# Optimization experiments

Hardware: AMD Instinct MI355X
Metric: run time of the kernel (lower is better)

## Reference

```python
import jax, jax.numpy as jnp
import numpy as np

B, S, E = 4, 4096, 1024
H, D, L = 16, 64, 64   # heads, head_dim, landmarks
KS = 33                # depthwise conv kernel size (seq dim)
N_ITER = 6


def setup_inputs() -> dict:
    key = jax.random.key(0)
    ks = jax.random.split(key, 8)
    s = 0.02
    return {
        "hidden_states": jax.random.normal(ks[0], (B, S, E), dtype=jnp.float32),
        "Wq": jax.random.normal(ks[1], (E, E), dtype=jnp.float32) * s,
        "bq": jnp.zeros((E,), dtype=jnp.float32),
        "Wk": jax.random.normal(ks[2], (E, E), dtype=jnp.float32) * s,
        "bk": jnp.zeros((E,), dtype=jnp.float32),
        "Wv": jax.random.normal(ks[3], (E, E), dtype=jnp.float32) * s,
        "bv": jnp.zeros((E,), dtype=jnp.float32),
        "conv_w": jax.random.normal(ks[4], (H, 1, KS, 1), dtype=jnp.float32) * 0.1,
    }


def _iterative_pinv_original(a, n_iter=N_ITER):
    # a: [B,H,L,L]. Faithful to _pinv_original_nystrom: GLOBAL max over all batches/heads.
    eye = jnp.eye(a.shape[-1], dtype=a.dtype)
    val = a.swapaxes(-1, -2) / jnp.max(jnp.sum(a, axis=-2))
    for _ in range(n_iter):
        kv = a @ val
        val = 0.25 * val @ (13.0 * eye - kv @ (15.0 * eye - kv @ (7.0 * eye - kv)))
    return val


def reference(hidden_states, Wq, bq, Wk, bk, Wv, bv, conv_w):
    scale = D ** -0.25  # divide q and k each by head_dim**0.25

    def heads(x):  # [B,S,E] -> [B,H,S,D]
        return x.reshape(B, S, H, D).transpose(0, 2, 1, 3)

    q = heads(hidden_states @ Wq + bq) * scale
    k = heads(hidden_states @ Wk + bk) * scale
    v = heads(hidden_states @ Wv + bv)

    # landmark means over segments of length S//L
    ql = q.reshape(B, H, L, S // L, D).mean(axis=-2)  # [B,H,L,D]
    kl = k.reshape(B, H, L, S // L, D).mean(axis=-2)  # [B,H,L,D]

    kernel_1 = jax.nn.softmax(jnp.einsum('bhsd,bhld->bhsl', q, kl), axis=-1)   # [B,H,S,L]
    kernel_2 = jax.nn.softmax(jnp.einsum('bhmd,bhld->bhml', ql, kl), axis=-1)  # [B,H,L,L]
    kernel_3 = jax.nn.softmax(jnp.einsum('bhld,bhsd->bhls', ql, k), axis=-1)   # [B,H,L,S]

    pinv = _iterative_pinv_original(kernel_2)
    attention_probs = kernel_1 @ pinv            # [B,H,S,L]
    new_value = kernel_3 @ v                     # [B,H,L,D]
    ctx = attention_probs @ new_value            # [B,H,S,D]

    # depthwise conv skip on value_layer: Conv2d(H,H,(KS,1),groups=H,bias=False)
    pad = KS // 2
    conv_out = jax.lax.conv_general_dilated(
        v, conv_w, window_strides=(1, 1), padding=((pad, pad), (0, 0)),
        dimension_numbers=('NCHW', 'OIHW', 'NCHW'), feature_group_count=H)
    ctx = ctx + conv_out

    return ctx.transpose(0, 2, 1, 3).reshape(B, S, H * D)
```

## Files before the change

### kernel.cpp

```cpp
#include <hip/hip_runtime.h>
#include <stdint.h>

typedef unsigned short u16;
typedef float f32x4 __attribute__((ext_vector_type(4)));
typedef __bf16 bf16x8 __attribute__((ext_vector_type(8)));
typedef u16 u16x8 __attribute__((ext_vector_type(8)));
typedef u16 u16x4 __attribute__((ext_vector_type(4)));

#define SCALE_QK 0.35355339059327373f

#define BAR() asm volatile("s_barrier" ::: "memory")
#define WAIT_LGKM0() do { asm volatile("s_waitcnt lgkmcnt(0)" ::: "memory"); __builtin_amdgcn_sched_barrier(0); } while (0)
#define WAIT_VM(n) do { asm volatile("s_waitcnt vmcnt(" #n ")" ::: "memory"); __builtin_amdgcn_sched_barrier(0); } while (0)

__device__ __forceinline__ u16 f2bf(float f) {
  union { float f; uint32_t u; } x; x.f = f;
  uint32_t r = x.u + 0x7fffu + ((x.u >> 16) & 1u);
  return (u16)(r >> 16);
}
__device__ __forceinline__ float bf2f(u16 h) {
  union { uint32_t u; float f; } x; x.u = ((uint32_t)h) << 16;
  return x.f;
}
__device__ __forceinline__ void gload16(const void* g, void* l) {
  __builtin_amdgcn_global_load_lds((const __attribute__((address_space(1))) void*)g,
                                   (__attribute__((address_space(3))) void*)l, 16, 0, 0);
}
__device__ __forceinline__ bf16x8 ld_f32_to_bf8(const float* p) {
  f32x4 a = *(const f32x4*)p, b = *(const f32x4*)(p + 4);
  union { u16x8 u; bf16x8 h; } c;
  c.u[0] = f2bf(a[0]); c.u[1] = f2bf(a[1]); c.u[2] = f2bf(a[2]); c.u[3] = f2bf(a[3]);
  c.u[4] = f2bf(b[0]); c.u[5] = f2bf(b[1]); c.u[6] = f2bf(b[2]); c.u[7] = f2bf(b[3]);
  return c.h;
}

__global__ __launch_bounds__(256) void k_wt(const float* __restrict__ Wq, const float* __restrict__ Wk,
                                            const float* __restrict__ Wv, u16* __restrict__ Wt) {
  __shared__ float tile[64][65];
  const int bx = blockIdx.x;
  const int w = bx >> 8, tn = (bx >> 4) & 15, tk = bx & 15;
  const float* W = (w == 0) ? Wq : ((w == 1) ? Wk : Wv);
  const int t = threadIdx.x;
  const int r = t >> 2, c0 = (t & 3) * 16;
  const float* src = W + (size_t)(tk * 64 + r) * 1024 + tn * 64 + c0;
#pragma unroll
  for (int j = 0; j < 16; j += 4) {
    f32x4 x = *(const f32x4*)(src + j);
    tile[r][c0 + j + 0] = x[0]; tile[r][c0 + j + 1] = x[1];
    tile[r][c0 + j + 2] = x[2]; tile[r][c0 + j + 3] = x[3];
  }
  __syncthreads();
  u16* dst = Wt + (size_t)(w * 1024 + tn * 64 + r) * 1024 + tk * 64 + c0;
#pragma unroll
  for (int j = 0; j < 16; ++j) dst[j] = f2bf(tile[c0 + j][r]);
}

__global__ __launch_bounds__(256) void k_hb(const float* __restrict__ in, u16* __restrict__ out) {
  const size_t i = ((size_t)blockIdx.x * 256 + threadIdx.x) * 8;
  f32x4 v0 = *(const f32x4*)(in + i);
  f32x4 v1 = *(const f32x4*)(in + i + 4);
  u16x8 o;
  o[0] = f2bf(v0[0]); o[1] = f2bf(v0[1]); o[2] = f2bf(v0[2]); o[3] = f2bf(v0[3]);
  o[4] = f2bf(v1[0]); o[5] = f2bf(v1[1]); o[6] = f2bf(v1[2]); o[7] = f2bf(v1[3]);
  *(u16x8*)(out + i) = o;
}

__device__ __forceinline__ bf16x8 frg(const u16* buf, int row, int ks, int lhi) {
  const int ck = (ks << 2) + lhi;
  return *reinterpret_cast<const bf16x8*>(buf + (row << 6) + ((ck ^ (row & 7)) << 3));
}
__device__ __forceinline__ void issue(const u16* g, int rowbase, int tc, u16* ldsbase, int wid) {
  gload16(g + (((size_t)rowbase) << 10) + tc, ldsbase + ((rowbase + (wid << 3)) << 6));
}
template <int Q>
__device__ __forceinline__ void quad_mfma(const bf16x8 (&af)[2][2], const bf16x8 (&bf)[4][2],
                                          f32x4 (&acc)[8][4]) {
#pragma unroll
  for (int mm = 0; mm < 2; ++mm)
#pragma unroll
    for (int n = 0; n < 4; ++n) {
      acc[Q * 2 + mm][n] = __builtin_amdgcn_mfma_f32_16x16x32_bf16(af[mm][0], bf[n][0], acc[Q * 2 + mm][n], 0, 0, 0);
      acc[Q * 2 + mm][n] = __builtin_amdgcn_mfma_f32_16x16x32_bf16(af[mm][1], bf[n][1], acc[Q * 2 + mm][n], 0, 0, 0);
    }
}
#define LOADA_TO(dst, Q)                                     \
  dst[0][0] = frg(ASr, rA0 + (Q)*32, 0, lhi);                \
  dst[0][1] = frg(ASr, rA0 + (Q)*32, 1, lhi);                \
  dst[1][0] = frg(ASr, rA0 + (Q)*32 + 16, 0, lhi);           \
  dst[1][1] = frg(ASr, rA0 + (Q)*32 + 16, 1, lhi);

__global__ __launch_bounds__(512) void k_gemm2(const u16* __restrict__ A, const u16* __restrict__ Bt,
                                               const float* __restrict__ bq, const float* __restrict__ bk,
                                               const float* __restrict__ bv,
                                               u16* __restrict__ oq, u16* __restrict__ ok, u16* __restrict__ ov,
                                               float* __restrict__ ql, float* __restrict__ kl) {
  __shared__ __align__(16) u16 AS[2][256 * 64];
  __shared__ __align__(16) u16 BS[2][256 * 64];
  __shared__ __align__(16) u16 obuf[8][16][70];
  const int t = threadIdx.x, lane = t & 63, wid = t >> 6;
  const int wm = wid >> 2, wn = wid & 3;
  const int bm = blockIdx.x, bn = blockIdx.y;
  const int l15 = lane & 15, lhi = lane >> 4;

  const int rowoff = t >> 3;
  const int cswz = (t & 7) ^ (rowoff & 7);
  const u16* aG = A + (((size_t)(bm * 256 + rowoff)) << 10) + (cswz << 3);
  const u16* bG = Bt + (((size_t)(bn * 256 + rowoff)) << 10) + (cswz << 3);

  const int rA0 = wm * 128 + l15;
  const int rB0 = wn * 64 + l15;

  f32x4 acc[8][4];
#pragma unroll
  for (int m = 0; m < 8; ++m)
#pragma unroll
    for (int n = 0; n < 4; ++n) acc[m][n] = (f32x4){0.f, 0.f, 0.f, 0.f};

  issue(bG, 0, 0, BS[0], wid);
  issue(bG, 64, 0, BS[0], wid);
  issue(bG, 128, 0, BS[0], wid);
  issue(bG, 192, 0, BS[0], wid);
  issue(aG, 0, 0, AS[0], wid);
  issue(aG, 128, 0, AS[0], wid);
  issue(aG, 64, 0, AS[0], wid);
  issue(aG, 192, 0, AS[0], wid);
  WAIT_VM(0);
  BAR();

  for (int u = 0; u < 15; ++u) {
    const int pu = u & 1;
    const u16* ASr = AS[pu];
    const u16* BSr = BS[pu];
    u16* ASw = AS[pu ^ 1];
    u16* BSw = BS[pu ^ 1];
    const int tc = (u + 1) << 6;
    bf16x8 bfr[4][2];
    bf16x8 afA[2][2], afB[2][2];
#pragma unroll
    for (int n = 0; n < 4; ++n) {
      bfr[n][0] = frg(BSr, rB0 + n * 16, 0, lhi);
      bfr[n][1] = frg(BSr, rB0 + n * 16, 1, lhi);
    }
    LOADA_TO(afA, 0)
    LOADA_TO(afB, 1)
    issue(bG, 0, tc, BSw, wid);
    issue(bG, 64, tc, BSw, wid);
    issue(bG, 128, tc, BSw, wid);
    issue(bG, 192, tc, BSw, wid);
    issue(aG, 0, tc, ASw, wid);
    issue(aG, 128, tc, ASw, wid);
    __builtin_amdgcn_s_setprio(1);
    quad_mfma<0>(afA, bfr, acc);
    __builtin_amdgcn_s_setprio(0);
    LOADA_TO(afA, 2)
    issue(aG, 64, tc, ASw, wid);
    issue(aG, 192, tc, ASw, wid);
    __builtin_amdgcn_s_setprio(1);
    quad_mfma<1>(afB, bfr, acc);
    __builtin_amdgcn_s_setprio(0);
    LOADA_TO(afB, 3)
    __builtin_amdgcn_s_setprio(1);
    quad_mfma<2>(afA, bfr, acc);
    __builtin_amdgcn_s_setprio(0);
    __builtin_amdgcn_s_setprio(1);
    quad_mfma<3>(afB, bfr, acc);
    __builtin_amdgcn_s_setprio(0);
    WAIT_VM(0);
    BAR();
  }
  {
    const u16* ASr = AS[1];
    const u16* BSr = BS[1];
    bf16x8 bfr[4][2];
    bf16x8 afA[2][2], afB[2][2];
#pragma unroll
    for (int n = 0; n < 4; ++n) {
      bfr[n][0] = frg(BSr, rB0 + n * 16, 0, lhi);
      bfr[n][1] = frg(BSr, rB0 + n * 16, 1, lhi);
    }
    LOADA_TO(afA, 0)
    LOADA_TO(afB, 1)
    quad_mfma<0>(afA, bfr, acc);
    LOADA_TO(afA, 2)
    quad_mfma<1>(afB, bfr, acc);
    LOADA_TO(afB, 3)
    quad_mfma<2>(afA, bfr, acc);
    quad_mfma<3>(afB, bfr, acc);
  }

  const int which = bn >> 2;
  const float* bias = (which == 0) ? bq : ((which == 1) ? bk : bv);
  u16* op = (which == 0) ? oq : ((which == 1) ? ok : ov);
  const float scl = (which < 2) ? SCALE_QK : 1.0f;
  const int h = ((bn & 3) << 2) + wn;
  const int rowBase2 = (bm << 8) + (wm << 7);
  const int rl = lhi << 2;
  const int srow = lane >> 2, d0 = (lane & 3) * 16;
  float bb[4];
#pragma unroll
  for (int n = 0; n < 4; ++n) bb[n] = bias[((bn & 3) << 8) + (wn << 6) + n * 16 + l15];
#pragma unroll
  for (int m = 0; m < 8; ++m) {
#pragma unroll
    for (int n = 0; n < 4; ++n)
#pragma unroll
      for (int r = 0; r < 4; ++r)
        obuf[wid][rl + r][n * 16 + l15] = f2bf((acc[m][n][r] + bb[n]) * scl);
    const int gm = rowBase2 + m * 16 + srow;
    const int b_ = gm >> 12, s = gm & 4095;
    u16* dst = op + (((size_t)b_ * 16 + h) * 4096 + s) * 64 + d0;
    *(u16x8*)dst = *(const u16x8*)&obuf[wid][srow][d0];
    *(u16x8*)(dst + 8) = *(const u16x8*)&obuf[wid][srow][d0 + 8];
  }
  if (which < 2) {
    float* lmp = (which == 0) ? ql : kl;
    const int bh = ((bm >> 4) << 4) + h;
#pragma unroll
    for (int sg = 0; sg < 2; ++sg) {
#pragma unroll
      for (int n = 0; n < 4; ++n) {
        float s = 0.f;
#pragma unroll
        for (int mi = 0; mi < 4; ++mi)
#pragma unroll
          for (int r = 0; r < 4; ++r) s += (acc[sg * 4 + mi][n][r] + bb[n]) * scl;
        s += __shfl_xor(s, 16, 64);
        s += __shfl_xor(s, 32, 64);
        if (lhi == 0) {
          const int lseg = ((bm & 15) << 2) + (wm << 1) + sg;
          lmp[(size_t)bh * 4096 + lseg * 64 + n * 16 + l15] = s * 0.015625f;
        }
      }
    }
  }
}

__global__ __launch_bounds__(256) void k_k2(const float* __restrict__ ql, const float* __restrict__ kl,
                                            float* __restrict__ k2t, float* __restrict__ colmax,
                                            u16* __restrict__ klb) {
  __shared__ __align__(16) float qlT[64 * 68];
  __shared__ __align__(16) float klT[64 * 68];
  __shared__ __align__(16) float sc[64 * 68];
  const int bh = blockIdx.x, t = threadIdx.x;
  {
    const int r = t >> 2, c0 = (t & 3) * 16;
    const float* qp = ql + (size_t)bh * 4096 + r * 64 + c0;
    const float* kp = kl + (size_t)bh * 4096 + r * 64 + c0;
    u16* kb_ = klb + (size_t)bh * 4096 + r * 64 + c0;
#pragma unroll
    for (int j = 0; j < 16; ++j) {
      qlT[(c0 + j) * 68 + r] = qp[j];
      const float kv = kp[j];
      klT[(c0 + j) * 68 + r] = kv;
      kb_[j] = f2bf(kv);
    }
  }
  __syncthreads();
  {
    const int mg = (t >> 4) * 4, lg = (t & 15) * 4;
    float acc[4][4];
#pragma unroll
    for (int i = 0; i < 4; ++i)
#pragma unroll
      for (int j = 0; j < 4; ++j) acc[i][j] = 0.f;
    for (int d0 = 0; d0 < 64; ++d0) {
      f32x4 x = *(const f32x4*)&qlT[d0 * 68 + mg];
      f32x4 y = *(const f32x4*)&klT[d0 * 68 + lg];
#pragma unroll
      for (int i = 0; i < 4; ++i)
#pragma unroll
        for (int j = 0; j < 4; ++j) acc[i][j] += x[i] * y[j];
    }
#pragma unroll
    for (int i = 0; i < 4; ++i)
#pragma unroll
      for (int j = 0; j < 4; ++j) sc[(mg + i) * 68 + lg + j] = acc[i][j];
  }
  __syncthreads();
  if (t < 64) {
    float mx = -1e30f;
    for (int l = 0; l < 64; ++l) mx = fmaxf(mx, sc[t * 68 + l]);
    float sum = 0.f;
    for (int l = 0; l < 64; ++l) { float e = __expf(sc[t * 68 + l] - mx); sc[t * 68 + l] = e; sum += e; }
    const float inv = 1.0f / sum;
    for (int l = 0; l < 64; ++l) sc[t * 68 + l] *= inv;
  }
  __syncthreads();
  {
    const int r = t >> 2, c0 = (t & 3) * 16;
    float* ot = k2t + (size_t)bh * 4096 + r * 64 + c0;
#pragma unroll
    for (int j = 0; j < 16; ++j) ot[j] = sc[(c0 + j) * 68 + r];
  }
  if (t < 64) {
    float s = 0.f;
    for (int m = 0; m < 64; ++m) s += sc[m * 68 + t];
    for (int off = 32; off; off >>= 1) s = fmaxf(s, __shfl_down(s, off, 64));
    if (t == 0) colmax[bh] = s;
  }
}

__global__ __launch_bounds__(64) void k_max(const float* __restrict__ colmax, float* __restrict__ gmax) {
  const int t = threadIdx.x;
  float v = colmax[t];
  for (int off = 32; off; off >>= 1) v = fmaxf(v, __shfl_down(v, off, 64));
  if (t == 0) *gmax = v;
}

__global__ __launch_bounds__(512) void k_pinv(const float* __restrict__ k2t, const float* __restrict__ gmaxp,
                                              float* __restrict__ pinv) {
  __shared__ float valN[4096];
  __shared__ float kvT[4096];
  __shared__ float t1N[4096];
  __shared__ float t2N[4096];
  const int bh = blockIdx.x, t = threadIdx.x;
  const float* aT = k2t + (size_t)bh * 4096;
  const float ginv = 1.0f / gmaxp[0];
  const int rt = t >> 3, ct0 = (t & 7) * 8;
  {
    const float* p = aT + rt * 64 + ct0;
#pragma unroll
    for (int j = 0; j < 8; ++j) valN[rt * 64 + ct0 + j] = p[j] * ginv;
  }
  __syncthreads();
  const int rg = (t >> 4) * 2, cg = (t & 15) * 4;
  float acc[2][4];
  for (int it = 0; it < 6; ++it) {
#pragma unroll
    for (int i = 0; i < 2; ++i)
#pragma unroll
      for (int j = 0; j < 4; ++j) acc[i][j] = 0.f;
    for (int k = 0; k < 64; ++k) {
      const float x0 = aT[k * 64 + rg], x1 = aT[k * 64 + rg + 1];
      f32x4 y = *(const f32x4*)&valN[k * 64 + cg];
#pragma unroll
      for (int j = 0; j < 4; ++j) { acc[0][j] += x0 * y[j]; acc[1][j] += x1 * y[j]; }
    }
#pragma unroll
    for (int i = 0; i < 2; ++i)
#pragma unroll
      for (int j = 0; j < 4; ++j) kvT[(cg + j) * 64 + rg + i] = acc[i][j];
    __syncthreads();
#pragma unroll
    for (int j = 0; j < 8; ++j) {
      const int c = ct0 + j;
      t1N[rt * 64 + c] = ((rt == c) ? 7.0f : 0.0f) - kvT[c * 64 + rt];
    }
    __syncthreads();
#pragma unroll
    for (int i = 0; i < 2; ++i)
#pragma unroll
      for (int j = 0; j < 4; ++j) acc[i][j] = 0.f;
    for (int k = 0; k < 64; ++k) {
      const float x0 = kvT[k * 64 + rg], x1 = kvT[k * 64 + rg + 1];
      f32x4 y = *(const f32x4*)&t1N[k * 64 + cg];
#pragma unroll
      for (int j = 0; j < 4; ++j) { acc[0][j] += x0 * y[j]; acc[1][j] += x1 * y[j]; }
    }
#pragma unroll
    for (int i = 0; i < 2; ++i)
#pragma unroll
      for (int j = 0; j < 4; ++j) {
        const int r_ = rg + i, c_ = cg + j;
        t2N[r_ * 64 + c_] = ((r_ == c_) ? 15.0f : 0.0f) - acc[i][j];
      }
    __syncthreads();
#pragma unroll
    for (int i = 0; i < 2; ++i)
#pragma unroll
      for (int j = 0; j < 4; ++j) acc[i][j] = 0.f;
    for (int k = 0; k < 64; ++k) {
      const float x0 = kvT[k * 64 + rg], x1 = kvT[k * 64 + rg + 1];
      f32x4 y = *(const f32x4*)&t2N[k * 64 + cg];
#pragma unroll
      for (int j = 0; j < 4; ++j) { acc[0][j] += x0 * y[j]; acc[1][j] += x1 * y[j]; }
    }
#pragma unroll
    for (int i = 0; i < 2; ++i)
#pragma unroll
      for (int j = 0; j < 4; ++j) {
        const int r_ = rg + i, c_ = cg + j;
        t1N[r_ * 64 + c_] = ((r_ == c_) ? 13.0f : 0.0f) - acc[i][j];
      }
    __syncthreads();
#pragma unroll
    for (int j = 0; j < 8; ++j) t2N[(ct0 + j) * 64 + rt] = valN[rt * 64 + ct0 + j];
    __syncthreads();
#pragma unroll
    for (int i = 0; i < 2; ++i)
#pragma unroll
      for (int j = 0; j < 4; ++j) acc[i][j] = 0.f;
    for (int k = 0; k < 64; ++k) {
      const float x0 = t2N[k * 64 + rg], x1 = t2N[k * 64 + rg + 1];
      f32x4 y = *(const f32x4*)&t1N[k * 64 + cg];
#pragma unroll
      for (int j = 0; j < 4; ++j) { acc[0][j] += x0 * y[j]; acc[1][j] += x1 * y[j]; }
    }
#pragma unroll
    for (int i = 0; i < 2; ++i)
#pragma unroll
      for (int j = 0; j < 4; ++j) valN[(rg + i) * 64 + cg + j] = 0.25f * acc[i][j];
    __syncthreads();
  }
  {
    float* o = pinv + (size_t)bh * 4096 + rt * 64 + ct0;
#pragma unroll
    for (int j = 0; j < 8; ++j) o[j] = valN[rt * 64 + ct0 + j];
  }
}

__global__ __launch_bounds__(256) void k_s3nv(const float* __restrict__ ql, const u16* __restrict__ kb,
                                              const u16* __restrict__ vb,
                                              float* __restrict__ nvp, float* __restrict__ zp) {
  __shared__ __align__(16) u16 VT[64][72];
  __shared__ __align__(16) u16 e_lds[4][16][72];
  const int bh = blockIdx.x, scn = blockIdx.y;
  const int t = threadIdx.x, lane = t & 63, w = t >> 6;
  const int l15 = lane & 15, kg = (lane >> 4) << 3, rl = (lane >> 4) << 2;
  const float* aRow = ql + (size_t)bh * 4096 + (w * 16 + l15) * 64 + kg;
  bf16x8 aql[2];
  aql[0] = ld_f32_to_bf8(aRow);
  aql[1] = ld_f32_to_bf8(aRow + 32);
  f32x4 accv[4];
#pragma unroll
  for (int n = 0; n < 4; ++n) accv[n] = (f32x4){0.f, 0.f, 0.f, 0.f};
  float zacc[4] = {0.f, 0.f, 0.f, 0.f};

  for (int sub = 0; sub < 16; ++sub) {
    const int s0 = scn * 1024 + sub * 64;
    __syncthreads();
    {
      const u16* vp = vb + ((size_t)bh * 4096 + s0 + lane) * 64 + w * 16;
      u16x8 h0 = *(const u16x8*)vp, h1 = *(const u16x8*)(vp + 8);
#pragma unroll
      for (int j = 0; j < 8; ++j) { VT[w * 16 + j][lane] = h0[j]; VT[w * 16 + 8 + j][lane] = h1[j]; }
    }
    __syncthreads();
    const u16* bRow = kb + ((size_t)bh * 4096 + s0 + l15) * 64 + kg;
    f32x4 e[4];
#pragma unroll
    for (int n = 0; n < 4; ++n) e[n] = (f32x4){0.f, 0.f, 0.f, 0.f};
#pragma unroll
    for (int ks = 0; ks < 2; ++ks)
#pragma unroll
      for (int n = 0; n < 4; ++n) {
        bf16x8 bk = *reinterpret_cast<const bf16x8*>(bRow + n * 1024 + ks * 32);
        e[n] = __builtin_amdgcn_mfma_f32_16x16x32_bf16(aql[ks], bk, e[n], 0, 0, 0);
      }
#pragma unroll
    for (int n = 0; n < 4; ++n)
#pragma unroll
      for (int r = 0; r < 4; ++r) {
        const float v = __expf(e[n][r]);
        zacc[r] += v;
        e_lds[w][rl + r][n * 16 + l15] = f2bf(v);
      }
    WAIT_LGKM0();
#pragma unroll
    for (int ks = 0; ks < 2; ++ks) {
      bf16x8 af = *reinterpret_cast<const bf16x8*>(&e_lds[w][l15][kg + ks * 32]);
#pragma unroll
      for (int n = 0; n < 4; ++n) {
        bf16x8 bf_ = *reinterpret_cast<const bf16x8*>(&VT[n * 16 + l15][kg + ks * 32]);
        accv[n] = __builtin_amdgcn_mfma_f32_16x16x32_bf16(af, bf_, accv[n], 0, 0, 0);
      }
    }
  }
#pragma unroll
  for (int r = 0; r < 4; ++r)
#pragma unroll
    for (int n = 0; n < 4; ++n)
      nvp[(((size_t)scn * 64 + bh) * 64 + w * 16 + rl + r) * 64 + n * 16 + l15] = accv[n][r];
#pragma unroll
  for (int r = 0; r < 4; ++r) {
    float s = zacc[r];
    s += __shfl_xor(s, 1, 64); s += __shfl_xor(s, 2, 64);
    s += __shfl_xor(s, 4, 64); s += __shfl_xor(s, 8, 64);
    if (l15 == 0) zp[((size_t)scn * 64 + bh) * 64 + w * 16 + rl + r] = s;
  }
}

__global__ __launch_bounds__(256) void k_pnv(const float* __restrict__ pinv, const float* __restrict__ nvp,
                                             const float* __restrict__ zp, u16* __restrict__ Mtb) {
  __shared__ __align__(16) float XT[64 * 68];
  __shared__ __align__(16) float Y[64 * 68];
  const int bh = blockIdx.x, t = threadIdx.x;
  {
    const int r = t >> 2, c0 = (t & 3) * 16;
    const float* pp = pinv + (size_t)bh * 4096 + r * 64 + c0;
#pragma unroll
    for (int j = 0; j < 16; ++j) XT[(c0 + j) * 68 + r] = pp[j];
    float zs = 0.f;
#pragma unroll
    for (int p = 0; p < 4; ++p) zs += zp[((size_t)p * 64 + bh) * 64 + r];
    const float iz = 1.0f / zs;
#pragma unroll
    for (int j = 0; j < 16; ++j) {
      float s = 0.f;
#pragma unroll
      for (int p = 0; p < 4; ++p) s += nvp[(((size_t)p * 64 + bh) * 64 + r) * 64 + c0 + j];
      Y[r * 68 + c0 + j] = s * iz;
    }
  }
  __syncthreads();
  const int rg = (t >> 4) * 4, cg = (t & 15) * 4;
  float acc[4][4];
#pragma unroll
  for (int i = 0; i < 4; ++i)
#pragma unroll
    for (int j = 0; j < 4; ++j) acc[i][j] = 0.f;
  for (int k = 0; k < 64; ++k) {
    f32x4 x = *(const f32x4*)&XT[k * 68 + rg];
    f32x4 y = *(const f32x4*)&Y[k * 68 + cg];
#pragma unroll
    for (int i = 0; i < 4; ++i)
#pragma unroll
      for (int j = 0; j < 4; ++j) acc[i][j] += x[i] * y[j];
  }
#pragma unroll
  for (int j = 0; j < 4; ++j) {
    u16x4 o = {f2bf(acc[0][j]), f2bf(acc[1][j]), f2bf(acc[2][j]), f2bf(acc[3][j])};
    *(u16x4*)&Mtb[(size_t)bh * 4096 + (cg + j) * 64 + rg] = o;
  }
}

__global__ __launch_bounds__(256) void k_out(const u16* __restrict__ qb, const u16* __restrict__ vb,
                                             const u16* __restrict__ klb, const u16* __restrict__ Mtb,
                                             const float* __restrict__ cw, float* __restrict__ out) {
  __shared__ __align__(16) u16 P_lds[4][16][72];
  __shared__ __align__(16) u16 vtile_t[64][100];
  __shared__ float wsh[33];
  const int bid = blockIdx.x;
  const int bh = bid >> 6, st = bid & 63;
  const int b = bh >> 4, h = bh & 15;
  const int t = threadIdx.x, lane = t & 63, w = t >> 6;
  const int sbase = st * 64;
  const int l15 = lane & 15, kg = (lane >> 4) << 3, rl = (lane >> 4) << 2;

  if (t < 33) wsh[t] = cw[h * 33 + t];
  for (int idx = t; idx < 96 * 8; idx += 256) {
    const int row = idx >> 3, c8 = idx & 7;
    const int sg = sbase + row - 16;
    u16x8 val = {0, 0, 0, 0, 0, 0, 0, 0};
    if (sg >= 0 && sg < 4096) val = *(const u16x8*)(vb + ((size_t)bh * 4096 + sg) * 64 + c8 * 8);
#pragma unroll
    for (int j = 0; j < 8; ++j) vtile_t[c8 * 8 + j][row] = val[j];
  }

  f32x4 c1[4];
#pragma unroll
  for (int n = 0; n < 4; ++n) c1[n] = (f32x4){0.f, 0.f, 0.f, 0.f};
  {
    const u16* aRow = qb + ((size_t)bh * 4096 + sbase + w * 16 + l15) * 64 + kg;
    const u16* kRow = klb + (size_t)bh * 4096 + l15 * 64 + kg;
#pragma unroll
    for (int ks = 0; ks < 2; ++ks) {
      bf16x8 af = *reinterpret_cast<const bf16x8*>(aRow + ks * 32);
#pragma unroll
      for (int n = 0; n < 4; ++n) {
        bf16x8 bf_ = *reinterpret_cast<const bf16x8*>(kRow + n * 1024 + ks * 32);
        c1[n] = __builtin_amdgcn_mfma_f32_16x16x32_bf16(af, bf_, c1[n], 0, 0, 0);
      }
    }
  }
  float invZ[4];
  {
    float z[4] = {0.f, 0.f, 0.f, 0.f};
#pragma unroll
    for (int n = 0; n < 4; ++n)
#pragma unroll
      for (int r = 0; r < 4; ++r) { float v = __expf(c1[n][r]); c1[n][r] = v; z[r] += v; }
#pragma unroll
    for (int r = 0; r < 4; ++r) {
      float s = z[r];
      s += __shfl_xor(s, 1, 64); s += __shfl_xor(s, 2, 64);
      s += __shfl_xor(s, 4, 64); s += __shfl_xor(s, 8, 64);
      invZ[r] = 1.0f / s;
    }
#pragma unroll
    for (int n = 0; n < 4; ++n)
#pragma unroll
      for (int r = 0; r < 4; ++r)
        P_lds[w][rl + r][n * 16 + l15] = f2bf(c1[n][r]);
  }
  __syncthreads();
  f32x4 c2[4];
#pragma unroll
  for (int n = 0; n < 4; ++n) c2[n] = (f32x4){0.f, 0.f, 0.f, 0.f};
  {
    const u16* mRow = Mtb + (size_t)bh * 4096 + l15 * 64 + kg;
#pragma unroll
    for (int ks = 0; ks < 2; ++ks) {
      bf16x8 af = *reinterpret_cast<const bf16x8*>(&P_lds[w][l15][kg + ks * 32]);
#pragma unroll
      for (int n = 0; n < 4; ++n) {
        bf16x8 bf_ = *reinterpret_cast<const bf16x8*>(mRow + n * 1024 + ks * 32);
        c2[n] = __builtin_amdgcn_mfma_f32_16x16x32_bf16(af, bf_, c2[n], 0, 0, 0);
      }
    }
  }
  const int base = w * 16 + rl;
#pragma unroll
  for (int n = 0; n < 4; ++n) {
    const int d = n * 16 + l15;
    float vcol[36];
#pragma unroll
    for (int k8 = 0; k8 < 9; ++k8) {
      u16x4 vq = *(const u16x4*)&vtile_t[d][base + k8 * 4];
      vcol[k8 * 4 + 0] = bf2f(vq[0]); vcol[k8 * 4 + 1] = bf2f(vq[1]);
      vcol[k8 * 4 + 2] = bf2f(vq[2]); vcol[k8 * 4 + 3] = bf2f(vq[3]);
    }
    float cv[4] = {0.f, 0.f, 0.f, 0.f};
#pragma unroll
    for (int jt = 0; jt < 33; ++jt) {
      const float ww = wsh[jt];
#pragma unroll
      for (int r = 0; r < 4; ++r) cv[r] += ww * vcol[r + jt];
    }
#pragma unroll
    for (int r = 0; r < 4; ++r) {
      const int sgl = sbase + base + r;
      out[((size_t)b * 4096 + sgl) * 1024 + h * 64 + d] = c2[n][r] * invZ[r] + cv[r];
    }
  }
}

extern "C" void kernel_launch(void* const* d_in, const int* in_sizes, int n_in,
                              void* d_out, int out_size, void* d_ws, size_t ws_size,
                              hipStream_t stream) {
  const float* hidden = (const float*)d_in[0];
  const float* Wq = (const float*)d_in[1];
  const float* bq = (const float*)d_in[2];
  const float* Wk = (const float*)d_in[3];
  const float* bk = (const float*)d_in[4];
  const float* Wv = (const float*)d_in[5];
  const float* bv = (const float*)d_in[6];
  const float* cw = (const float*)d_in[7];
  float* out = (float*)d_out;

  char* ws = (char*)d_ws;
  u16* qb = (u16*)(ws);
  u16* kb = (u16*)(ws + 33554432ull);
  u16* vb = (u16*)(ws + 67108864ull);
  float* ql = (float*)(ws + 100663296ull);
  float* kl = (float*)(ws + 101711872ull);
  float* k2t = (float*)(ws + 102760448ull);
  float* pinvb = (float*)(ws + 103809024ull);
  float* nvp = (float*)(ws + 104857600ull);
  float* zp = (float*)(ws + 109051904ull);
  u16* Mtb = (u16*)(ws + 109117440ull);
  u16* klb = (u16*)(ws + 109641728ull);
  float* stats = (float*)(ws + 110690304ull);
  u16* wt = (u16*)(ws + 110694400ull);
  u16* hb = (u16*)(ws + 116985856ull);

  k_wt<<<768, 256, 0, stream>>>(Wq, Wk, Wv, wt);
  k_hb<<<8192, 256, 0, stream>>>(hidden, hb);
  k_gemm2<<<dim3(64, 12), 512, 0, stream>>>(hb, wt, bq, bk, bv, qb, kb, vb, ql, kl);
  k_k2<<<64, 256, 0, stream>>>(ql, kl, k2t, stats, klb);
  k_max<<<1, 64, 0, stream>>>(stats, stats + 64);
  k_pinv<<<64, 512, 0, stream>>>(k2t, stats + 64, pinvb);
  k_s3nv<<<dim3(64, 4), 256, 0, stream>>>(ql, kb, vb, nvp, zp);
  k_pnv<<<64, 256, 0, stream>>>(pinvb, nvp, zp, Mtb);
  k_out<<<4096, 256, 0, stream>>>(qb, vb, klb, Mtb, cw, out);
  (void)in_sizes; (void)n_in; (void)out_size; (void)ws_size;
}
```

Baseline: 307.2 us.

## Fuse prep kernels, fold max into pinv, deepen GEMM pipelining, split s3nv wider

Merges the weight transpose and hidden-state bf16 conversion into a single launch, and folds the global-max reduction into the pinv kernel, which removes two kernel launches. The GEMM main loop now issues all A-tile loads up front and waits on partial vmcnt with an extra mid-iteration barrier, so loads overlap more with MFMA work. k_s3nv is split over twice as many sequence chunks, and each block double-buffers its V tile with a register prefetch. The extra barrier and the reuse of the hb workspace for nvp add risk: the aliasing is only safe if hb is no longer read when k_s3nv runs.

```diff
diff --git a/kernel.cpp b/kernel.cpp
--- a/kernel.cpp
+++ b/kernel.cpp
@@ -34,13 +34,26 @@
   return c.h;
 }
 
-__global__ __launch_bounds__(256) void k_wt(const float* __restrict__ Wq, const float* __restrict__ Wk,
-                                            const float* __restrict__ Wv, u16* __restrict__ Wt) {
+__global__ __launch_bounds__(256) void k_prep(const float* __restrict__ hidden,
+                                              const float* __restrict__ Wq, const float* __restrict__ Wk,
+                                              const float* __restrict__ Wv,
+                                              u16* __restrict__ hb, u16* __restrict__ Wt) {
   __shared__ float tile[64][65];
   const int bx = blockIdx.x;
-  const int w = bx >> 8, tn = (bx >> 4) & 15, tk = bx & 15;
+  const int t = threadIdx.x;
+  if (bx < 8192) {
+    const size_t i = ((size_t)bx * 256 + t) * 8;
+    f32x4 v0 = *(const f32x4*)(hidden + i);
+    f32x4 v1 = *(const f32x4*)(hidden + i + 4);
+    u16x8 o;
+    o[0] = f2bf(v0[0]); o[1] = f2bf(v0[1]); o[2] = f2bf(v0[2]); o[3] = f2bf(v0[3]);
+    o[4] = f2bf(v1[0]); o[5] = f2bf(v1[1]); o[6] = f2bf(v1[2]); o[7] = f2bf(v1[3]);
+    *(u16x8*)(hb + i) = o;
+    return;
+  }
+  const int bxx = bx - 8192;
+  const int w = bxx >> 8, tn = (bxx >> 4) & 15, tk = bxx & 15;
   const float* W = (w == 0) ? Wq : ((w == 1) ? Wk : Wv);
-  const int t = threadIdx.x;
   const int r = t >> 2, c0 = (t & 3) * 16;
   const float* src = W + (size_t)(tk * 64 + r) * 1024 + tn * 64 + c0;
 #pragma unroll
@@ -53,16 +66,6 @@
   u16* dst = Wt + (size_t)(w * 1024 + tn * 64 + r) * 1024 + tk * 64 + c0;
 #pragma unroll
   for (int j = 0; j < 16; ++j) dst[j] = f2bf(tile[c0 + j][r]);
-}
-
-__global__ __launch_bounds__(256) void k_hb(const float* __restrict__ in, u16* __restrict__ out) {
-  const size_t i = ((size_t)blockIdx.x * 256 + threadIdx.x) * 8;
-  f32x4 v0 = *(const f32x4*)(in + i);
-  f32x4 v1 = *(const f32x4*)(in + i + 4);
-  u16x8 o;
-  o[0] = f2bf(v0[0]); o[1] = f2bf(v0[1]); o[2] = f2bf(v0[2]); o[3] = f2bf(v0[3]);
-  o[4] = f2bf(v1[0]); o[5] = f2bf(v1[1]); o[6] = f2bf(v1[2]); o[7] = f2bf(v1[3]);
-  *(u16x8*)(out + i) = o;
 }
 
 __device__ __forceinline__ bf16x8 frg(const u16* buf, int row, int ks, int lhi) {
@@ -124,7 +127,7 @@
   issue(aG, 128, 0, AS[0], wid);
   issue(aG, 64, 0, AS[0], wid);
   issue(aG, 192, 0, AS[0], wid);
-  WAIT_VM(0);
+  WAIT_VM(2);
   BAR();
 
   for (int u = 0; u < 15; ++u) {
@@ -149,12 +152,14 @@
     issue(bG, 192, tc, BSw, wid);
     issue(aG, 0, tc, ASw, wid);
     issue(aG, 128, tc, ASw, wid);
+    issue(aG, 64, tc, ASw, wid);
+    issue(aG, 192, tc, ASw, wid);
     __builtin_amdgcn_s_setprio(1);
     quad_mfma<0>(afA, bfr, acc);
     __builtin_amdgcn_s_setprio(0);
+    WAIT_VM(8);
+    BAR();
     LOADA_TO(afA, 2)
-    issue(aG, 64, tc, ASw, wid);
-    issue(aG, 192, tc, ASw, wid);
     __builtin_amdgcn_s_setprio(1);
     quad_mfma<1>(afB, bfr, acc);
     __builtin_amdgcn_s_setprio(0);
@@ -165,7 +170,7 @@
     __builtin_amdgcn_s_setprio(1);
     quad_mfma<3>(afB, bfr, acc);
     __builtin_amdgcn_s_setprio(0);
-    WAIT_VM(0);
+    WAIT_VM(2);
     BAR();
   }
   {
@@ -181,6 +186,8 @@
     LOADA_TO(afA, 0)
     LOADA_TO(afB, 1)
     quad_mfma<0>(afA, bfr, acc);
+    WAIT_VM(0);
+    BAR();
     LOADA_TO(afA, 2)
     quad_mfma<1>(afB, bfr, acc);
     LOADA_TO(afB, 3)
@@ -300,22 +307,22 @@
   }
 }
 
-__global__ __launch_bounds__(64) void k_max(const float* __restrict__ colmax, float* __restrict__ gmax) {
-  const int t = threadIdx.x;
-  float v = colmax[t];
-  for (int off = 32; off; off >>= 1) v = fmaxf(v, __shfl_down(v, off, 64));
-  if (t == 0) *gmax = v;
-}
-
-__global__ __launch_bounds__(512) void k_pinv(const float* __restrict__ k2t, const float* __restrict__ gmaxp,
+__global__ __launch_bounds__(512) void k_pinv(const float* __restrict__ k2t, const float* __restrict__ colmax,
                                               float* __restrict__ pinv) {
   __shared__ float valN[4096];
   __shared__ float kvT[4096];
   __shared__ float t1N[4096];
   __shared__ float t2N[4096];
+  __shared__ float gsh;
   const int bh = blockIdx.x, t = threadIdx.x;
   const float* aT = k2t + (size_t)bh * 4096;
-  const float ginv = 1.0f / gmaxp[0];
+  if (t < 64) {
+    float v = colmax[t];
+    for (int off = 32; off; off >>= 1) v = fmaxf(v, __shfl_down(v, off, 64));
+    if (t == 0) gsh = v;
+  }
+  __syncthreads();
+  const float ginv = 1.0f / gsh;
   const int rt = t >> 3, ct0 = (t & 7) * 8;
   {
     const float* p = aT + rt * 64 + ct0;
@@ -412,7 +419,7 @@
 __global__ __launch_bounds__(256) void k_s3nv(const float* __restrict__ ql, const u16* __restrict__ kb,
                                               const u16* __restrict__ vb,
                                               float* __restrict__ nvp, float* __restrict__ zp) {
-  __shared__ __align__(16) u16 VT[64][72];
+  __shared__ __align__(16) u16 VT[2][64][72];
   __shared__ __align__(16) u16 e_lds[4][16][72];
   const int bh = blockIdx.x, scn = blockIdx.y;
   const int t = threadIdx.x, lane = t & 63, w = t >> 6;
@@ -425,17 +432,21 @@
 #pragma unroll
   for (int n = 0; n < 4; ++n) accv[n] = (f32x4){0.f, 0.f, 0.f, 0.f};
   float zacc[4] = {0.f, 0.f, 0.f, 0.f};
-
-  for (int sub = 0; sub < 16; ++sub) {
-    const int s0 = scn * 1024 + sub * 64;
-    __syncthreads();
-    {
-      const u16* vp = vb + ((size_t)bh * 4096 + s0 + lane) * 64 + w * 16;
-      u16x8 h0 = *(const u16x8*)vp, h1 = *(const u16x8*)(vp + 8);
-#pragma unroll
-      for (int j = 0; j < 8; ++j) { VT[w * 16 + j][lane] = h0[j]; VT[w * 16 + 8 + j][lane] = h1[j]; }
-    }
-    __syncthreads();
+  const int sBase = scn * 512;
+  {
+    const u16* vp = vb + ((size_t)bh * 4096 + sBase + lane) * 64 + w * 16;
+    u16x8 h0 = *(const u16x8*)vp, h1 = *(const u16x8*)(vp + 8);
+#pragma unroll
+    for (int j = 0; j < 8; ++j) { VT[0][w * 16 + j][lane] = h0[j]; VT[0][w * 16 + 8 + j][lane] = h1[j]; }
+  }
+  __syncthreads();
+  for (int sub = 0; sub < 8; ++sub) {
+    const int s0 = sBase + sub * 64;
+    u16x8 hn0 = {0,0,0,0,0,0,0,0}, hn1 = {0,0,0,0,0,0,0,0};
+    if (sub < 7) {
+      const u16* vpn = vb + ((size_t)bh * 4096 + s0 + 64 + lane) * 64 + w * 16;
+      hn0 = *(const u16x8*)vpn; hn1 = *(const u16x8*)(vpn + 8);
+    }
     const u16* bRow = kb + ((size_t)bh * 4096 + s0 + l15) * 64 + kg;
     f32x4 e[4];
 #pragma unroll
@@ -455,16 +466,23 @@
         zacc[r] += v;
         e_lds[w][rl + r][n * 16 + l15] = f2bf(v);
       }
+    if (sub < 7) {
+      const int nb = (sub + 1) & 1;
+#pragma unroll
+      for (int j = 0; j < 8; ++j) { VT[nb][w * 16 + j][lane] = hn0[j]; VT[nb][w * 16 + 8 + j][lane] = hn1[j]; }
+    }
     WAIT_LGKM0();
+    const int cb = sub & 1;
 #pragma unroll
     for (int ks = 0; ks < 2; ++ks) {
       bf16x8 af = *reinterpret_cast<const bf16x8*>(&e_lds[w][l15][kg + ks * 32]);
 #pragma unroll
       for (int n = 0; n < 4; ++n) {
-        bf16x8 bf_ = *reinterpret_cast<const bf16x8*>(&VT[n * 16 + l15][kg + ks * 32]);
+        bf16x8 bf_ = *reinterpret_cast<const bf16x8*>(&VT[cb][n * 16 + l15][kg + ks * 32]);
         accv[n] = __builtin_amdgcn_mfma_f32_16x16x32_bf16(af, bf_, accv[n], 0, 0, 0);
       }
     }
+    BAR();
   }
 #pragma unroll
   for (int r = 0; r < 4; ++r)
@@ -492,13 +510,13 @@
     for (int j = 0; j < 16; ++j) XT[(c0 + j) * 68 + r] = pp[j];
     float zs = 0.f;
 #pragma unroll
-    for (int p = 0; p < 4; ++p) zs += zp[((size_t)p * 64 + bh) * 64 + r];
+    for (int p = 0; p < 8; ++p) zs += zp[((size_t)p * 64 + bh) * 64 + r];
     const float iz = 1.0f / zs;
 #pragma unroll
     for (int j = 0; j < 16; ++j) {
       float s = 0.f;
 #pragma unroll
-      for (int p = 0; p < 4; ++p) s += nvp[(((size_t)p * 64 + bh) * 64 + r) * 64 + c0 + j];
+      for (int p = 0; p < 8; ++p) s += nvp[(((size_t)p * 64 + bh) * 64 + r) * 64 + c0 + j];
       Y[r * 68 + c0 + j] = s * iz;
     }
   }
@@ -646,21 +664,19 @@
   float* kl = (float*)(ws + 101711872ull);
   float* k2t = (float*)(ws + 102760448ull);
   float* pinvb = (float*)(ws + 103809024ull);
-  float* nvp = (float*)(ws + 104857600ull);
-  float* zp = (float*)(ws + 109051904ull);
-  u16* Mtb = (u16*)(ws + 109117440ull);
-  u16* klb = (u16*)(ws + 109641728ull);
-  float* stats = (float*)(ws + 110690304ull);
-  u16* wt = (u16*)(ws + 110694400ull);
-  u16* hb = (u16*)(ws + 116985856ull);
-
-  k_wt<<<768, 256, 0, stream>>>(Wq, Wk, Wv, wt);
-  k_hb<<<8192, 256, 0, stream>>>(hidden, hb);
+  u16* Mtb = (u16*)(ws + 104857600ull);
+  u16* klb = (u16*)(ws + 105381888ull);
+  float* stats = (float*)(ws + 106430464ull);
+  u16* wt = (u16*)(ws + 106434560ull);
+  u16* hb = (u16*)(ws + 112726016ull);
+  float* nvp = (float*)(ws + 112726016ull);
+  float* zp = (float*)(ws + 121114624ull);
+
+  k_prep<<<8960, 256, 0, stream>>>(hidden, Wq, Wk, Wv, hb, wt);
   k_gemm2<<<dim3(64, 12), 512, 0, stream>>>(hb, wt, bq, bk, bv, qb, kb, vb, ql, kl);
   k_k2<<<64, 256, 0, stream>>>(ql, kl, k2t, stats, klb);
-  k_max<<<1, 64, 0, stream>>>(stats, stats + 64);
-  k_pinv<<<64, 512, 0, stream>>>(k2t, stats + 64, pinvb);
-  k_s3nv<<<dim3(64, 4), 256, 0, stream>>>(ql, kb, vb, nvp, zp);
+  k_pinv<<<64, 512, 0, stream>>>(k2t, stats, pinvb);
+  k_s3nv<<<dim3(64, 8), 256, 0, stream>>>(ql, kb, vb, nvp, zp);
   k_pnv<<<64, 256, 0, stream>>>(pinvb, nvp, zp, Mtb);
   k_out<<<4096, 256, 0, stream>>>(qb, vb, klb, Mtb, cw, out);
   (void)in_sizes; (void)n_in; (void)out_size; (void)ws_size;
```

Result: faster. 298.1 us (-2.9%).
